# Kernel tuning notes

Measured on AMD Instinct MI355X. Metric: run time of the kernel, lower is better.

The kernel has to match this reference:

```python
import jax, jax.numpy as jnp
import numpy as np

LBL = 20            # original label_size
T = LBL + 2         # +START/+STOP for CRF
START = T - 2
STOP = T - 1
B, S, V, E, H = 64, 256, 50000, 300, 256


def setup_inputs() -> dict:
    key = jax.random.key(0)
    ks = jax.random.split(key, 20)
    s = 0.05
    inp = {
        "word_input": jax.random.randint(ks[0], (B, S), 0, V),
        "input_mask": jnp.ones((B, S), dtype=jnp.int32),
        "labels": jax.random.randint(ks[1], (B, S), 0, LBL),
        "labels_token": jax.random.randint(ks[2], (B, S), 0, 2),
        "emb_table": jax.random.normal(ks[3], (V, E)) * s,
        # PyTorch LSTM gate order: i, f, g, o (stacked along dim 0 of W)
        "Wih_f": jax.random.normal(ks[4], (4 * H, E)) * s,
        "Whh_f": jax.random.normal(ks[5], (4 * H, H)) * s,
        "bih_f": jax.random.normal(ks[6], (4 * H,)) * s,
        "bhh_f": jax.random.normal(ks[7], (4 * H,)) * s,
        "Wih_b": jax.random.normal(ks[8], (4 * H, E)) * s,
        "Whh_b": jax.random.normal(ks[9], (4 * H, H)) * s,
        "bih_b": jax.random.normal(ks[10], (4 * H,)) * s,
        "bhh_b": jax.random.normal(ks[11], (4 * H,)) * s,
        "W_tag": jax.random.normal(ks[12], (T, 2 * H)) * s,
        "b_tag": jax.random.normal(ks[13], (T,)) * s,
        "W_tok": jax.random.normal(ks[14], (2, 2 * H)) * s,
        "b_tok": jax.random.normal(ks[15], (2,)) * s,
        "trans": jax.random.normal(ks[16], (T, T)) * 0.1,
    }
    return inp


def _lstm_dir(x, Wih, Whh, bih, bhh, reverse):
    # x: [B, S, E] -> hs: [B, S, H]
    b = x.shape[0]
    h0 = jnp.zeros((b, Whh.shape[1]), x.dtype)

    def step(carry, xt):
        h, c = carry
        g = xt @ Wih.T + bih + h @ Whh.T + bhh
        i, f, gg, o = jnp.split(g, 4, axis=-1)
        c = jax.nn.sigmoid(f) * c + jax.nn.sigmoid(i) * jnp.tanh(gg)
        h = jax.nn.sigmoid(o) * jnp.tanh(c)
        return (h, c), h

    _, hs = jax.lax.scan(step, (h0, h0), jnp.swapaxes(x, 0, 1), reverse=reverse)
    return jnp.swapaxes(hs, 0, 1)


def _crf_nll(feats, mask, tags, trans):
    # feats: [B,S,T], mask: [B,S] int, tags: [B,S]
    maskf = mask.astype(feats.dtype)
    feats_t = jnp.swapaxes(feats, 0, 1)  # [S,B,T]
    mask_t = jnp.swapaxes(mask, 0, 1)
    part0 = feats_t[0] + trans[START][None]  # [B,T]

    def step(part, inputs):
        ft, mt = inputs
        newp = jax.nn.logsumexp(part[:, :, None] + trans[None], axis=1) + ft
        return jnp.where(mt[:, None] > 0, newp, part), None

    part, _ = jax.lax.scan(step, part0, (feats_t[1:], mask_t[1:]))
    fwd = jax.nn.logsumexp(part + trans[:, STOP][None], axis=1).sum()

    prev = jnp.concatenate(
        [jnp.full((tags.shape[0], 1), START, dtype=tags.dtype), tags[:, :-1]], axis=1)
    emit = jnp.take_along_axis(feats, tags[:, :, None], axis=2)[:, :, 0]
    gold = ((emit + trans[prev, tags]) * maskf).sum()
    lengths = mask.sum(axis=1)
    last_tag = jnp.take_along_axis(tags, (lengths - 1)[:, None], axis=1)[:, 0]
    gold = gold + trans[last_tag, STOP].sum()
    return fwd - gold


def _viterbi(feats, mask, trans):
    feats_t = jnp.swapaxes(feats, 0, 1)
    mask_t = jnp.swapaxes(mask, 0, 1)
    vit0 = feats_t[0] + trans[START][None]  # [B,T]
    idT = jnp.arange(T)

    def step(vit, inputs):
        ft, mt = inputs
        sc = vit[:, :, None] + trans[None]       # [B, T_prev, T_cur]
        bp = jnp.argmax(sc, axis=1)
        newv = jnp.max(sc, axis=1) + ft
        vit = jnp.where(mt[:, None] > 0, newv, vit)
        bp = jnp.where(mt[:, None] > 0, bp, idT[None])  # identity at padding
        return vit, bp

    vit, bps = jax.lax.scan(step, vit0, (feats_t[1:], mask_t[1:]))  # bps: [S-1,B,T]
    final = vit + trans[:, STOP][None]
    score = jnp.max(final, axis=1)
    last = jnp.argmax(final, axis=1)

    def back(tag, bp):
        prev = jnp.take_along_axis(bp, tag[:, None], axis=1)[:, 0]
        return prev, prev

    _, prevs = jax.lax.scan(back, last, bps, reverse=True)  # [S-1,B]
    tags = jnp.concatenate([prevs, last[None]], axis=0)      # [S,B]
    return score, jnp.swapaxes(tags, 0, 1)


def reference(word_input, input_mask, labels, labels_token, emb_table,
              Wih_f, Whh_f, bih_f, bhh_f, Wih_b, Whh_b, bih_b, bhh_b,
              W_tag, b_tag, W_tok, b_tok, trans):
    x = emb_table[word_input]                                  # [B,S,E]
    x = x * input_mask[:, :, None].astype(x.dtype)
    h_f = _lstm_dir(x, Wih_f, Whh_f, bih_f, bhh_f, reverse=False)
    h_b = _lstm_dir(x, Wih_b, Whh_b, bih_b, bhh_b, reverse=True)
    output = jnp.concatenate([h_f, h_b], axis=-1)              # [B,S,2H]

    tag_feats = output @ W_tag.T + b_tag                       # [B,S,T]
    tok_logits = output @ W_tok.T + b_tok                      # [B,S,2]

    # token CE: active positions (mask==1) and ignore_index=0
    logp = jax.nn.log_softmax(tok_logits, axis=-1)
    ce = -jnp.take_along_axis(logp, labels_token[:, :, None], axis=2)[:, :, 0]
    w = ((input_mask == 1) & (labels_token != 0)).astype(ce.dtype)
    token_loss = (ce * w).sum() / jnp.maximum(w.sum(), 1.0)

    nll = _crf_nll(tag_feats, input_mask, labels, trans)
    scores, tag_seq = _viterbi(tag_feats, input_mask, trans)
    ans_loss = nll / word_input.shape[0] + token_loss
    return ans_loss, tag_seq
```

## Files before the change

kernel.cpp:

```cpp
#include <hip/hip_runtime.h>
#include <math.h>

typedef unsigned short u16;
typedef unsigned int u32;

#define NB 64
#define NS 256
#define NE 300
#define NH 256
#define NT 22
#define KPAD 304
#define NBS (NB*NS)
#define START_TAG 20
#define STOP_TAG 21

#define RKC 20
#define LDSC 9
#define SKC 35

typedef float f32x4 __attribute__((ext_vector_type(4)));

__device__ __forceinline__ float fsig(float x) {
    return 1.f / (1.f + expf(-x));
}

__global__ __launch_bounds__(128) void gather_ax(const int* __restrict__ word,
                                                 const int* __restrict__ mask,
                                                 const float* __restrict__ emb,
                                                 float* __restrict__ Ax) {
    int bs = blockIdx.x;
    int t = threadIdx.x;
    if (t >= 76) return;
    int w = word[bs];
    int m = mask[bs];
    f32x4 v = {0.f, 0.f, 0.f, 0.f};
    if (t < 75 && m != 0) v = *(const f32x4*)(emb + (size_t)w * NE + t * 4);
    *(f32x4*)(Ax + (size_t)bs * KPAD + t * 4) = v;
}

__global__ __launch_bounds__(64) void pack_wih(const float* __restrict__ Wf, const float* __restrict__ Wb,
                                               const float* __restrict__ bihf, const float* __restrict__ bhhf,
                                               const float* __restrict__ bihb, const float* __restrict__ bhhb,
                                               float* __restrict__ WihP, float* __restrict__ biasP) {
    int j = blockIdx.x & 1023;
    int dir = blockIdx.x >> 10;
    const float* W = dir ? Wb : Wf;
    for (int k = threadIdx.x; k < KPAD; k += 64)
        WihP[((size_t)dir * 1024 + j) * KPAD + k] = (k < NE) ? W[(size_t)j * NE + k] : 0.f;
    if (threadIdx.x == 0) {
        const float* b1 = dir ? bihb : bihf;
        const float* b2 = dir ? bhhb : bhhf;
        biasP[dir * 1024 + j] = b1[j] + b2[j];
    }
}

__global__ __launch_bounds__(256) void pack_wstream(const float* __restrict__ Whf,
                                                    const float* __restrict__ Whb,
                                                    float* __restrict__ Wst) {
    int idx = blockIdx.x * 256 + threadIdx.x;
    int dir = idx / (SKC * 1024);
    int r = idx % (SKC * 1024);
    int cc = r >> 10;
    int row = r & 1023;
    const float* W = dir ? Whb : Whf;
    f32x4 v = *(const f32x4*)(W + (size_t)row * NH + 4 * (RKC + LDSC + cc));
    *((f32x4*)Wst + idx) = v;
}

__global__ __launch_bounds__(256) void gemm_xproj(const float* __restrict__ Ax,
                                                  const float* __restrict__ WihP,
                                                  const float* __restrict__ biasP,
                                                  float* __restrict__ Xp) {
    int m0 = blockIdx.x * 128;
    int n0 = blockIdx.y * 64;
    int dir = blockIdx.z;
    const float* Bsrc = WihP + (size_t)dir * 1024 * KPAD;
    __shared__ float Asm[16][132];
    __shared__ float Bsm[16][68];
    int tid = threadIdx.x;
    int arow = tid >> 1;
    int acol = (tid & 1) * 8;
    int brow = tid >> 2;
    int bcol = (tid & 3) * 4;
    int ty = tid >> 4;
    int tx = tid & 15;
    float acc[8][4] = {};

    for (int ks = 0; ks < KPAD / 16; ++ks) {
        int k0 = ks * 16;
        f32x4 ga0 = *(const f32x4*)(Ax + (size_t)(m0 + arow) * KPAD + k0 + acol);
        f32x4 ga1 = *(const f32x4*)(Ax + (size_t)(m0 + arow) * KPAD + k0 + acol + 4);
        f32x4 gb = *(const f32x4*)(Bsrc + (size_t)(n0 + brow) * KPAD + k0 + bcol);
        __syncthreads();
#pragma unroll
        for (int j = 0; j < 4; ++j) {
            Asm[acol + j][arow] = ga0[j];
            Asm[acol + 4 + j][arow] = ga1[j];
            Bsm[bcol + j][brow] = gb[j];
        }
        __syncthreads();
#pragma unroll
        for (int k = 0; k < 16; ++k) {
            f32x4 a0 = *(const f32x4*)&Asm[k][ty * 8];
            f32x4 a1 = *(const f32x4*)&Asm[k][ty * 8 + 4];
            f32x4 b4 = *(const f32x4*)&Bsm[k][tx * 4];
#pragma unroll
            for (int i = 0; i < 4; ++i)
#pragma unroll
                for (int j = 0; j < 4; ++j) {
                    acc[i][j] = fmaf(a0[i], b4[j], acc[i][j]);
                    acc[i + 4][j] = fmaf(a1[i], b4[j], acc[i + 4][j]);
                }
        }
    }
    f32x4 bv = *(const f32x4*)(biasP + dir * 1024 + n0 + tx * 4);
#pragma unroll
    for (int i = 0; i < 8; ++i) {
        f32x4 o;
#pragma unroll
        for (int j = 0; j < 4; ++j) o[j] = acc[i][j] + bv[j];
        *(f32x4*)(Xp + ((size_t)dir * NBS + m0 + ty * 8 + i) * 1024 + n0 + tx * 4) = o;
    }
}

__global__ __launch_bounds__(1024, 4) void lstm5(const float* __restrict__ Xp,
                                                 const float* __restrict__ Whf,
                                                 const float* __restrict__ Whb,
                                                 const float* __restrict__ Wst,
                                                 float* __restrict__ hbuf) {
    int bid = blockIdx.x;
    int dir = bid >> 6;
    int b = bid & 63;
    int tid = threadIdx.x;
    int gate = tid >> 8;
    int j = tid & 255;
    __shared__ f32x4 wlds[LDSC][1024];
    __shared__ float h_sh[256];
    __shared__ float exch[3][256];

    const float* W = dir ? Whb : Whf;
    const f32x4* wrow = (const f32x4*)(W + (size_t)tid * NH);
    const f32x4* ws = (const f32x4*)Wst + (size_t)dir * SKC * 1024;

    f32x4 wr[RKC];
#pragma unroll
    for (int i = 0; i < RKC; ++i) wr[i] = wrow[i];
#pragma unroll
    for (int i = 0; i < LDSC; ++i) wlds[i][tid] = wrow[RKC + i];

    const float* X = Xp + ((size_t)dir * NBS + (size_t)b * NS) * 1024;
    float* Hout = hbuf + ((size_t)dir * NBS + (size_t)b * NS) * NH;
    const f32x4* hs4 = (const f32x4*)h_sh;
    float c = 0.f;
    if (gate == 0) h_sh[j] = 0.f;
    __syncthreads();

    for (int t = 0; t < NS; ++t) {
        int s = dir ? (NS - 1 - t) : t;
        float acc = X[(size_t)s * 1024 + tid];
#pragma unroll 5
        for (int cc = 0; cc < SKC; ++cc) {
            f32x4 wv = ws[(size_t)cc * 1024 + tid];
            f32x4 hq = hs4[RKC + LDSC + cc];
            acc = fmaf(wv[0], hq[0], fmaf(wv[1], hq[1], fmaf(wv[2], hq[2], fmaf(wv[3], hq[3], acc))));
        }
#pragma unroll
        for (int i = 0; i < RKC; ++i) {
            f32x4 hq = hs4[i];
            acc = fmaf(wr[i][0], hq[0], fmaf(wr[i][1], hq[1], fmaf(wr[i][2], hq[2], fmaf(wr[i][3], hq[3], acc))));
        }
#pragma unroll
        for (int i = 0; i < LDSC; ++i) {
            f32x4 wv = wlds[i][tid];
            f32x4 hq = hs4[RKC + i];
            acc = fmaf(wv[0], hq[0], fmaf(wv[1], hq[1], fmaf(wv[2], hq[2], fmaf(wv[3], hq[3], acc))));
        }
        if (gate) exch[gate - 1][j] = (gate == 2) ? tanhf(acc) : fsig(acc);
        __syncthreads();
        if (!gate) {
            float gi = fsig(acc);
            float gf = exch[0][j];
            float gg = exch[1][j];
            float oo = exch[2][j];
            c = gf * c + gi * gg;
            float h = oo * tanhf(c);
            h_sh[j] = h;
            Hout[(size_t)s * NH + j] = h;
        }
        __syncthreads();
    }
}

__global__ __launch_bounds__(256) void feats_kernel(const float* __restrict__ hbuf,
                                                    const float* __restrict__ Wtag, const float* __restrict__ btag,
                                                    const float* __restrict__ Wtok, const float* __restrict__ btok,
                                                    const int* __restrict__ mask, const int* __restrict__ ltok,
                                                    float* __restrict__ feats,
                                                    float* __restrict__ ce_arr, float* __restrict__ cnt_arr) {
    int gw = (blockIdx.x * 256 + threadIdx.x) >> 6;
    int lane = threadIdx.x & 63;
    float ce = 0.f, cnt = 0.f;
    for (int i = 0; i < 8; ++i) {
        int bs = gw * 8 + i;
        size_t base = (lane < 32) ? ((size_t)bs * NH + lane * 8)
                                  : ((size_t)NBS * NH + (size_t)bs * NH + (lane - 32) * 8);
        f32x4 v0 = *(const f32x4*)(hbuf + base);
        f32x4 v1 = *(const f32x4*)(hbuf + base + 4);
        float vals[8] = {v0[0], v0[1], v0[2], v0[3], v1[0], v1[1], v1[2], v1[3]};
        float t0 = 0.f, t1 = 0.f;
        for (int u = 0; u < 24; ++u) {
            const float* wr = (u < NT) ? (Wtag + (size_t)u * 512) : (Wtok + (size_t)(u - NT) * 512);
            f32x4 w0 = *(const f32x4*)(wr + lane * 8);
            f32x4 w1 = *(const f32x4*)(wr + lane * 8 + 4);
            float d = vals[0] * w0[0] + vals[1] * w0[1] + vals[2] * w0[2] + vals[3] * w0[3]
                    + vals[4] * w1[0] + vals[5] * w1[1] + vals[6] * w1[2] + vals[7] * w1[3];
#pragma unroll
            for (int o = 32; o; o >>= 1) d += __shfl_xor(d, o);
            if (u < NT) {
                if (lane == 0) feats[(size_t)bs * 24 + u] = d + btag[u];
            } else if (u == NT) {
                t0 = d + btok[0];
            } else {
                t1 = d + btok[1];
            }
        }
        if (lane == 0) {
            float m = fmaxf(t0, t1);
            float lse = m + logf(expf(t0 - m) + expf(t1 - m));
            int lab = ltok[bs];
            int mk = mask[bs];
            if (mk == 1 && lab != 0) {
                ce += lse - (lab ? t1 : t0);
                cnt += 1.f;
            }
        }
    }
    if (lane == 0) { ce_arr[gw] = ce; cnt_arr[gw] = cnt; }
}

__global__ __launch_bounds__(64) void crf_kernel(const float* __restrict__ feats,
                                                 const int* __restrict__ mask,
                                                 const int* __restrict__ labels,
                                                 const float* __restrict__ trans,
                                                 float* __restrict__ contrib,
                                                 float* __restrict__ outtags) {
    int b = blockIdx.x, t = threadIdx.x;
    __shared__ float tr[NT * NT];
    __shared__ float part_sh[NT], vit_sh[NT];
    __shared__ float red[NT];
    __shared__ unsigned char bp[NS][NT];
    for (int i = t; i < NT * NT; i += 64) tr[i] = trans[i];
    __syncthreads();
    const float* F = feats + (size_t)b * NS * 24;
    const int* Mrow = mask + b * NS;
    const int* Lrow = labels + b * NS;
    float part = 0.f, vit = 0.f;
    if (t < NT) {
        part = F[t] + tr[START_TAG * NT + t];
        vit = part;
        part_sh[t] = part;
        vit_sh[t] = vit;
    }
    __syncthreads();
    for (int s = 1; s < NS; ++s) {
        float newp = part, newv = vit;
        int bi = t;
        if (t < NT) {
            float ft = F[s * 24 + t];
            float mx = -1e30f;
#pragma unroll
            for (int p = 0; p < NT; ++p) mx = fmaxf(mx, part_sh[p] + tr[p * NT + t]);
            float sm = 0.f;
#pragma unroll
            for (int p = 0; p < NT; ++p) sm += expf(part_sh[p] + tr[p * NT + t] - mx);
            float cp = mx + logf(sm) + ft;
            float bm = -1e30f;
            int bj = 0;
#pragma unroll
            for (int p = 0; p < NT; ++p) {
                float sc = vit_sh[p] + tr[p * NT + t];
                if (sc > bm) { bm = sc; bj = p; }
            }
            float cv = bm + ft;
            if (Mrow[s] > 0) { newp = cp; newv = cv; bi = bj; }
        }
        __syncthreads();
        if (t < NT) {
            part = newp; vit = newv;
            part_sh[t] = part; vit_sh[t] = vit;
            bp[s][t] = (unsigned char)bi;
        }
        __syncthreads();
    }
    float val = (t < NT) ? part + tr[t * NT + STOP_TAG] : -1e30f;
    float mx = val;
#pragma unroll
    for (int o = 32; o; o >>= 1) mx = fmaxf(mx, __shfl_xor(mx, o));
    float ex = (t < NT) ? expf(val - mx) : 0.f;
#pragma unroll
    for (int o = 32; o; o >>= 1) ex += __shfl_xor(ex, o);
    float fwd = mx + logf(ex);
    if (t < NT) red[t] = vit + tr[t * NT + STOP_TAG];
    __syncthreads();
    if (t == 0) {
        float bm = -1e30f;
        int bi = 0;
        for (int p = 0; p < NT; ++p)
            if (red[p] > bm) { bm = red[p]; bi = p; }
        int cur = bi;
        outtags[b * NS + NS - 1] = (float)cur;
        for (int s = NS - 1; s >= 1; --s) {
            cur = bp[s][cur];
            outtags[b * NS + s - 1] = (float)cur;
        }
    }
    float g = 0.f;
    int len = 0;
    for (int s = t; s < NS; s += 64) {
        int tg = Lrow[s];
        int pv = (s == 0) ? START_TAG : Lrow[s - 1];
        if (Mrow[s] > 0) {
            g += F[s * 24 + tg] + tr[pv * NT + tg];
            len += 1;
        }
    }
#pragma unroll
    for (int o = 32; o; o >>= 1) { g += __shfl_xor(g, o); len += __shfl_xor(len, o); }
    if (t == 0) {
        int lt = Lrow[len - 1];
        g += tr[lt * NT + STOP_TAG];
        contrib[b] = fwd - g;
    }
}

__global__ __launch_bounds__(256) void finalize_kernel(const float* __restrict__ contrib,
                                                       const float* __restrict__ ce_arr,
                                                       const float* __restrict__ cnt_arr,
                                                       float* __restrict__ out) {
    __shared__ float sA[256], sB[256], sC[256];
    int t = threadIdx.x;
    float a = (t < NB) ? contrib[t] : 0.f;
    float bb = 0.f, cc = 0.f;
    for (int i = t; i < 2048; i += 256) { bb += ce_arr[i]; cc += cnt_arr[i]; }
    sA[t] = a; sB[t] = bb; sC[t] = cc;
    __syncthreads();
    for (int o = 128; o; o >>= 1) {
        if (t < o) { sA[t] += sA[t + o]; sB[t] += sB[t + o]; sC[t] += sC[t + o]; }
        __syncthreads();
    }
    if (t == 0)
        out[0] = sA[0] / (float)NB + sB[0] / fmaxf(sC[0], 1.f);
}

extern "C" void kernel_launch(void* const* d_in, const int* in_sizes, int n_in,
                              void* d_out, int out_size, void* d_ws, size_t ws_size,
                              hipStream_t stream) {
    const int*   word   = (const int*)d_in[0];
    const int*   mask   = (const int*)d_in[1];
    const int*   labels = (const int*)d_in[2];
    const int*   ltok   = (const int*)d_in[3];
    const float* emb    = (const float*)d_in[4];
    const float* Wih_f  = (const float*)d_in[5];
    const float* Whh_f  = (const float*)d_in[6];
    const float* bih_f  = (const float*)d_in[7];
    const float* bhh_f  = (const float*)d_in[8];
    const float* Wih_b  = (const float*)d_in[9];
    const float* Whh_b  = (const float*)d_in[10];
    const float* bih_b  = (const float*)d_in[11];
    const float* bhh_b  = (const float*)d_in[12];
    const float* Wtag   = (const float*)d_in[13];
    const float* btag   = (const float*)d_in[14];
    const float* Wtok   = (const float*)d_in[15];
    const float* btok   = (const float*)d_in[16];
    const float* trans  = (const float*)d_in[17];
    float* out = (float*)d_out;

    char* ws = (char*)d_ws;
    size_t off = 0;
    auto alloc = [&](size_t bytes) { size_t r = off; off += (bytes + 255) & ~(size_t)255; return r; };
    float* Ax     = (float*)(ws + alloc((size_t)NBS * KPAD * 4));
    float* WihP   = (float*)(ws + alloc((size_t)2 * 1024 * KPAD * 4));
    float* biasP  = (float*)(ws + alloc((size_t)2 * 1024 * 4));
    float* Wst    = (float*)(ws + alloc((size_t)2 * SKC * 1024 * 16));
    float* Xp     = (float*)(ws + alloc((size_t)2 * NBS * 1024 * 4));
    float* hbuf   = (float*)(ws + alloc((size_t)2 * NBS * NH * 4));
    float* feats  = (float*)(ws + alloc((size_t)NBS * 24 * 4));
    float* contrib= (float*)(ws + alloc((size_t)NB * 4));
    float* ce_arr = (float*)(ws + alloc((size_t)2048 * 4));
    float* cnt_arr= (float*)(ws + alloc((size_t)2048 * 4));

    gather_ax<<<NBS, 128, 0, stream>>>(word, mask, emb, Ax);
    pack_wih<<<2048, 64, 0, stream>>>(Wih_f, Wih_b, bih_f, bhh_f, bih_b, bhh_b, WihP, biasP);
    pack_wstream<<<(2 * SKC * 1024) / 256, 256, 0, stream>>>(Whh_f, Whh_b, Wst);
    gemm_xproj<<<dim3(NBS / 128, 1024 / 64, 2), 256, 0, stream>>>(Ax, WihP, biasP, Xp);
    lstm5<<<128, 1024, 0, stream>>>(Xp, Whh_f, Whh_b, Wst, hbuf);
    feats_kernel<<<512, 256, 0, stream>>>(hbuf, Wtag, btag, Wtok, btok, mask, ltok, feats, ce_arr, cnt_arr);
    crf_kernel<<<NB, 64, 0, stream>>>(feats, mask, labels, trans, contrib, out + 1);
    finalize_kernel<<<1, 256, 0, stream>>>(contrib, ce_arr, cnt_arr, out);
}
```

Before: 2.246 ms.

## Fuse embedding gather into input GEMM and repack recurrent weights chunk-major

Removes the separate embedding gather kernel and its padded intermediate buffer: the input-projection GEMM now reads embedding rows directly, applying the mask and zero padding as it loads. The recurrent weights are repacked fully chunk-major so every per-thread load in the LSTM is coalesced. The register/stream split is shifted (fewer register chunks, more streamed chunks), with an asm barrier pinning the weights in VGPRs and a smaller unroll. The trade is more streamed weight traffic per timestep in the sequential LSTM loop, in exchange for lower register pressure and one fewer launch.

```diff
diff --git a/kernel.cpp b/kernel.cpp
--- a/kernel.cpp
+++ b/kernel.cpp
@@ -14,28 +14,14 @@
 #define START_TAG 20
 #define STOP_TAG 21
 
-#define RKC 20
+#define RKC 18
 #define LDSC 9
-#define SKC 35
+#define SKC 37
 
 typedef float f32x4 __attribute__((ext_vector_type(4)));
 
 __device__ __forceinline__ float fsig(float x) {
     return 1.f / (1.f + expf(-x));
-}
-
-__global__ __launch_bounds__(128) void gather_ax(const int* __restrict__ word,
-                                                 const int* __restrict__ mask,
-                                                 const float* __restrict__ emb,
-                                                 float* __restrict__ Ax) {
-    int bs = blockIdx.x;
-    int t = threadIdx.x;
-    if (t >= 76) return;
-    int w = word[bs];
-    int m = mask[bs];
-    f32x4 v = {0.f, 0.f, 0.f, 0.f};
-    if (t < 75 && m != 0) v = *(const f32x4*)(emb + (size_t)w * NE + t * 4);
-    *(f32x4*)(Ax + (size_t)bs * KPAD + t * 4) = v;
 }
 
 __global__ __launch_bounds__(64) void pack_wih(const float* __restrict__ Wf, const float* __restrict__ Wb,
@@ -54,20 +40,22 @@
     }
 }
 
-__global__ __launch_bounds__(256) void pack_wstream(const float* __restrict__ Whf,
-                                                    const float* __restrict__ Whb,
-                                                    float* __restrict__ Wst) {
+__global__ __launch_bounds__(256) void pack_wall(const float* __restrict__ Whf,
+                                                 const float* __restrict__ Whb,
+                                                 float* __restrict__ WstAll) {
     int idx = blockIdx.x * 256 + threadIdx.x;
-    int dir = idx / (SKC * 1024);
-    int r = idx % (SKC * 1024);
+    int dir = idx >> 16;
+    int r = idx & 65535;
     int cc = r >> 10;
     int row = r & 1023;
     const float* W = dir ? Whb : Whf;
-    f32x4 v = *(const f32x4*)(W + (size_t)row * NH + 4 * (RKC + LDSC + cc));
-    *((f32x4*)Wst + idx) = v;
-}
-
-__global__ __launch_bounds__(256) void gemm_xproj(const float* __restrict__ Ax,
+    f32x4 v = *(const f32x4*)(W + (size_t)row * NH + 4 * cc);
+    *((f32x4*)WstAll + idx) = v;
+}
+
+__global__ __launch_bounds__(256) void gemm_xproj(const int* __restrict__ word,
+                                                  const int* __restrict__ maskp,
+                                                  const float* __restrict__ emb,
                                                   const float* __restrict__ WihP,
                                                   const float* __restrict__ biasP,
                                                   float* __restrict__ Xp) {
@@ -86,10 +74,17 @@
     int tx = tid & 15;
     float acc[8][4] = {};
 
+    int bs = m0 + arow;
+    int wi = word[bs];
+    int mk = maskp[bs];
+    const float* erow = emb + (size_t)wi * NE;
+
     for (int ks = 0; ks < KPAD / 16; ++ks) {
         int k0 = ks * 16;
-        f32x4 ga0 = *(const f32x4*)(Ax + (size_t)(m0 + arow) * KPAD + k0 + acol);
-        f32x4 ga1 = *(const f32x4*)(Ax + (size_t)(m0 + arow) * KPAD + k0 + acol + 4);
+        int c0 = k0 + acol;
+        f32x4 ga0 = {0.f, 0.f, 0.f, 0.f}, ga1 = {0.f, 0.f, 0.f, 0.f};
+        if (mk && c0 < NE)     ga0 = *(const f32x4*)(erow + c0);
+        if (mk && c0 + 4 < NE) ga1 = *(const f32x4*)(erow + c0 + 4);
         f32x4 gb = *(const f32x4*)(Bsrc + (size_t)(n0 + brow) * KPAD + k0 + bcol);
         __syncthreads();
 #pragma unroll
@@ -123,10 +118,8 @@
     }
 }
 
-__global__ __launch_bounds__(1024, 4) void lstm5(const float* __restrict__ Xp,
-                                                 const float* __restrict__ Whf,
-                                                 const float* __restrict__ Whb,
-                                                 const float* __restrict__ Wst,
+__global__ __launch_bounds__(1024, 4) void lstm6(const float* __restrict__ Xp,
+                                                 const float* __restrict__ WstAll,
                                                  float* __restrict__ hbuf) {
     int bid = blockIdx.x;
     int dir = bid >> 6;
@@ -138,16 +131,18 @@
     __shared__ float h_sh[256];
     __shared__ float exch[3][256];
 
-    const float* W = dir ? Whb : Whf;
-    const f32x4* wrow = (const f32x4*)(W + (size_t)tid * NH);
-    const f32x4* ws = (const f32x4*)Wst + (size_t)dir * SKC * 1024;
+    const f32x4* wall = (const f32x4*)WstAll + (size_t)dir * 64 * 1024;
 
     f32x4 wr[RKC];
 #pragma unroll
-    for (int i = 0; i < RKC; ++i) wr[i] = wrow[i];
-#pragma unroll
-    for (int i = 0; i < LDSC; ++i) wlds[i][tid] = wrow[RKC + i];
-
+    for (int i = 0; i < RKC; ++i) wr[i] = wall[(size_t)i * 1024 + tid];
+#pragma unroll
+    for (int i = 0; i < RKC; ++i)
+        asm volatile("" : "+v"(wr[i][0]), "+v"(wr[i][1]), "+v"(wr[i][2]), "+v"(wr[i][3]));
+#pragma unroll
+    for (int i = 0; i < LDSC; ++i) wlds[i][tid] = wall[(size_t)(RKC + i) * 1024 + tid];
+
+    const f32x4* ws = wall + (size_t)(RKC + LDSC) * 1024;
     const float* X = Xp + ((size_t)dir * NBS + (size_t)b * NS) * 1024;
     float* Hout = hbuf + ((size_t)dir * NBS + (size_t)b * NS) * NH;
     const f32x4* hs4 = (const f32x4*)h_sh;
@@ -158,7 +153,7 @@
     for (int t = 0; t < NS; ++t) {
         int s = dir ? (NS - 1 - t) : t;
         float acc = X[(size_t)s * 1024 + tid];
-#pragma unroll 5
+#pragma unroll 4
         for (int cc = 0; cc < SKC; ++cc) {
             f32x4 wv = ws[(size_t)cc * 1024 + tid];
             f32x4 hq = hs4[RKC + LDSC + cc];
@@ -378,10 +373,9 @@
     char* ws = (char*)d_ws;
     size_t off = 0;
     auto alloc = [&](size_t bytes) { size_t r = off; off += (bytes + 255) & ~(size_t)255; return r; };
-    float* Ax     = (float*)(ws + alloc((size_t)NBS * KPAD * 4));
     float* WihP   = (float*)(ws + alloc((size_t)2 * 1024 * KPAD * 4));
     float* biasP  = (float*)(ws + alloc((size_t)2 * 1024 * 4));
-    float* Wst    = (float*)(ws + alloc((size_t)2 * SKC * 1024 * 16));
+    float* WstAll = (float*)(ws + alloc((size_t)2 * 64 * 1024 * 16));
     float* Xp     = (float*)(ws + alloc((size_t)2 * NBS * 1024 * 4));
     float* hbuf   = (float*)(ws + alloc((size_t)2 * NBS * NH * 4));
     float* feats  = (float*)(ws + alloc((size_t)NBS * 24 * 4));
@@ -389,11 +383,10 @@
     float* ce_arr = (float*)(ws + alloc((size_t)2048 * 4));
     float* cnt_arr= (float*)(ws + alloc((size_t)2048 * 4));
 
-    gather_ax<<<NBS, 128, 0, stream>>>(word, mask, emb, Ax);
     pack_wih<<<2048, 64, 0, stream>>>(Wih_f, Wih_b, bih_f, bhh_f, bih_b, bhh_b, WihP, biasP);
-    pack_wstream<<<(2 * SKC * 1024) / 256, 256, 0, stream>>>(Whh_f, Whh_b, Wst);
-    gemm_xproj<<<dim3(NBS / 128, 1024 / 64, 2), 256, 0, stream>>>(Ax, WihP, biasP, Xp);
-    lstm5<<<128, 1024, 0, stream>>>(Xp, Whh_f, Whh_b, Wst, hbuf);
+    pack_wall<<<512, 256, 0, stream>>>(Whh_f, Whh_b, WstAll);
+    gemm_xproj<<<dim3(NBS / 128, 1024 / 64, 2), 256, 0, stream>>>(word, mask, emb, WihP, biasP, Xp);
+    lstm6<<<128, 1024, 0, stream>>>(Xp, WstAll, hbuf);
     feats_kernel<<<512, 256, 0, stream>>>(hbuf, Wtag, btag, Wtok, btok, mask, ltok, feats, ce_arr, cnt_arr);
     crf_kernel<<<NB, 64, 0, stream>>>(feats, mask, labels, trans, contrib, out + 1);
     finalize_kernel<<<1, 256, 0, stream>>>(contrib, ce_arr, cnt_arr, out);
```

After: 2.379 ms. 1.06x slower.

## Fuse embedding gather into input GEMM, enlarge tile, sync-free wave-per-batch CRF

Applied to the files above, without the earlier changes.

Removes the separate embedding gather kernel and its intermediate buffer by loading embedding rows directly inside the input-projection GEMM, with masking and K padding handled in-kernel. The GEMM tile is widened to 128x128 so each thread computes 8x8 outputs, giving more reuse per shared-memory load. The CRF/Viterbi kernel now assigns one wavefront per batch row, four per block, and drops block-level barriers in the sequential recurrence. It relies on intra-wavefront lockstep for correctness of the shared-memory updates.

```diff
diff --git a/kernel.cpp b/kernel.cpp
--- a/kernel.cpp
+++ b/kernel.cpp
@@ -22,20 +22,6 @@
 
 __device__ __forceinline__ float fsig(float x) {
     return 1.f / (1.f + expf(-x));
-}
-
-__global__ __launch_bounds__(128) void gather_ax(const int* __restrict__ word,
-                                                 const int* __restrict__ mask,
-                                                 const float* __restrict__ emb,
-                                                 float* __restrict__ Ax) {
-    int bs = blockIdx.x;
-    int t = threadIdx.x;
-    if (t >= 76) return;
-    int w = word[bs];
-    int m = mask[bs];
-    f32x4 v = {0.f, 0.f, 0.f, 0.f};
-    if (t < 75 && m != 0) v = *(const f32x4*)(emb + (size_t)w * NE + t * 4);
-    *(f32x4*)(Ax + (size_t)bs * KPAD + t * 4) = v;
 }
 
 __global__ __launch_bounds__(64) void pack_wih(const float* __restrict__ Wf, const float* __restrict__ Wb,
@@ -67,59 +53,74 @@
     *((f32x4*)Wst + idx) = v;
 }
 
-__global__ __launch_bounds__(256) void gemm_xproj(const float* __restrict__ Ax,
-                                                  const float* __restrict__ WihP,
-                                                  const float* __restrict__ biasP,
-                                                  float* __restrict__ Xp) {
+__global__ __launch_bounds__(256, 4) void gemm_xproj(const int* __restrict__ word,
+                                                     const int* __restrict__ maskp,
+                                                     const float* __restrict__ emb,
+                                                     const float* __restrict__ WihP,
+                                                     const float* __restrict__ biasP,
+                                                     float* __restrict__ Xp) {
     int m0 = blockIdx.x * 128;
-    int n0 = blockIdx.y * 64;
+    int n0 = blockIdx.y * 128;
     int dir = blockIdx.z;
     const float* Bsrc = WihP + (size_t)dir * 1024 * KPAD;
     __shared__ float Asm[16][132];
-    __shared__ float Bsm[16][68];
+    __shared__ float Bsm[16][132];
     int tid = threadIdx.x;
     int arow = tid >> 1;
     int acol = (tid & 1) * 8;
-    int brow = tid >> 2;
-    int bcol = (tid & 3) * 4;
     int ty = tid >> 4;
     int tx = tid & 15;
-    float acc[8][4] = {};
+    float acc[8][8] = {};
+
+    int bs = m0 + arow;
+    int wi = word[bs];
+    int mk = maskp[bs];
+    const float* erow = emb + (size_t)wi * NE;
 
     for (int ks = 0; ks < KPAD / 16; ++ks) {
         int k0 = ks * 16;
-        f32x4 ga0 = *(const f32x4*)(Ax + (size_t)(m0 + arow) * KPAD + k0 + acol);
-        f32x4 ga1 = *(const f32x4*)(Ax + (size_t)(m0 + arow) * KPAD + k0 + acol + 4);
-        f32x4 gb = *(const f32x4*)(Bsrc + (size_t)(n0 + brow) * KPAD + k0 + bcol);
+        int c0 = k0 + acol;
+        f32x4 ga0 = {0.f, 0.f, 0.f, 0.f}, ga1 = {0.f, 0.f, 0.f, 0.f};
+        if (mk && c0 < NE)     ga0 = *(const f32x4*)(erow + c0);
+        if (mk && c0 + 4 < NE) ga1 = *(const f32x4*)(erow + c0 + 4);
+        f32x4 gb0 = *(const f32x4*)(Bsrc + (size_t)(n0 + arow) * KPAD + c0);
+        f32x4 gb1 = *(const f32x4*)(Bsrc + (size_t)(n0 + arow) * KPAD + c0 + 4);
         __syncthreads();
 #pragma unroll
         for (int j = 0; j < 4; ++j) {
             Asm[acol + j][arow] = ga0[j];
             Asm[acol + 4 + j][arow] = ga1[j];
-            Bsm[bcol + j][brow] = gb[j];
+            Bsm[acol + j][arow] = gb0[j];
+            Bsm[acol + 4 + j][arow] = gb1[j];
         }
         __syncthreads();
 #pragma unroll
         for (int k = 0; k < 16; ++k) {
             f32x4 a0 = *(const f32x4*)&Asm[k][ty * 8];
             f32x4 a1 = *(const f32x4*)&Asm[k][ty * 8 + 4];
-            f32x4 b4 = *(const f32x4*)&Bsm[k][tx * 4];
+            f32x4 b0 = *(const f32x4*)&Bsm[k][tx * 8];
+            f32x4 b1 = *(const f32x4*)&Bsm[k][tx * 8 + 4];
 #pragma unroll
             for (int i = 0; i < 4; ++i)
 #pragma unroll
                 for (int j = 0; j < 4; ++j) {
-                    acc[i][j] = fmaf(a0[i], b4[j], acc[i][j]);
-                    acc[i + 4][j] = fmaf(a1[i], b4[j], acc[i + 4][j]);
+                    acc[i][j]         = fmaf(a0[i], b0[j], acc[i][j]);
+                    acc[i][j + 4]     = fmaf(a0[i], b1[j], acc[i][j + 4]);
+                    acc[i + 4][j]     = fmaf(a1[i], b0[j], acc[i + 4][j]);
+                    acc[i + 4][j + 4] = fmaf(a1[i], b1[j], acc[i + 4][j + 4]);
                 }
         }
     }
-    f32x4 bv = *(const f32x4*)(biasP + dir * 1024 + n0 + tx * 4);
+    f32x4 bv0 = *(const f32x4*)(biasP + dir * 1024 + n0 + tx * 8);
+    f32x4 bv1 = *(const f32x4*)(biasP + dir * 1024 + n0 + tx * 8 + 4);
 #pragma unroll
     for (int i = 0; i < 8; ++i) {
-        f32x4 o;
-#pragma unroll
-        for (int j = 0; j < 4; ++j) o[j] = acc[i][j] + bv[j];
-        *(f32x4*)(Xp + ((size_t)dir * NBS + m0 + ty * 8 + i) * 1024 + n0 + tx * 4) = o;
+        f32x4 o0, o1;
+#pragma unroll
+        for (int j = 0; j < 4; ++j) { o0[j] = acc[i][j] + bv0[j]; o1[j] = acc[i][j + 4] + bv1[j]; }
+        float* dst = Xp + ((size_t)dir * NBS + m0 + ty * 8 + i) * 1024 + n0 + tx * 8;
+        *(f32x4*)dst = o0;
+        *(f32x4*)(dst + 4) = o1;
     }
 }
 
@@ -238,59 +239,57 @@
     if (lane == 0) { ce_arr[gw] = ce; cnt_arr[gw] = cnt; }
 }
 
-__global__ __launch_bounds__(64) void crf_kernel(const float* __restrict__ feats,
-                                                 const int* __restrict__ mask,
-                                                 const int* __restrict__ labels,
-                                                 const float* __restrict__ trans,
-                                                 float* __restrict__ contrib,
-                                                 float* __restrict__ outtags) {
-    int b = blockIdx.x, t = threadIdx.x;
+__global__ __launch_bounds__(256) void crf_kernel(const float* __restrict__ feats,
+                                                  const int* __restrict__ mask,
+                                                  const int* __restrict__ labels,
+                                                  const float* __restrict__ trans,
+                                                  float* __restrict__ contrib,
+                                                  float* __restrict__ outtags) {
+    int wid = threadIdx.x >> 6;
+    int lane = threadIdx.x & 63;
+    int b = blockIdx.x * 4 + wid;
     __shared__ float tr[NT * NT];
-    __shared__ float part_sh[NT], vit_sh[NT];
-    __shared__ float red[NT];
-    __shared__ unsigned char bp[NS][NT];
-    for (int i = t; i < NT * NT; i += 64) tr[i] = trans[i];
+    __shared__ float ps[4][NT], vs[4][NT];
+    __shared__ unsigned char bp[4][NS][NT];
+    for (int i = threadIdx.x; i < NT * NT; i += 256) tr[i] = trans[i];
     __syncthreads();
+
     const float* F = feats + (size_t)b * NS * 24;
     const int* Mrow = mask + b * NS;
     const int* Lrow = labels + b * NS;
+    int t = lane;
     float part = 0.f, vit = 0.f;
     if (t < NT) {
         part = F[t] + tr[START_TAG * NT + t];
         vit = part;
-        part_sh[t] = part;
-        vit_sh[t] = vit;
-    }
-    __syncthreads();
+        ps[wid][t] = part;
+        vs[wid][t] = vit;
+    }
     for (int s = 1; s < NS; ++s) {
-        float newp = part, newv = vit;
-        int bi = t;
+        int mt = Mrow[s];
         if (t < NT) {
             float ft = F[s * 24 + t];
-            float mx = -1e30f;
-#pragma unroll
-            for (int p = 0; p < NT; ++p) mx = fmaxf(mx, part_sh[p] + tr[p * NT + t]);
+            float mx = -1e30f, bm = -1e30f;
+            int bj = 0;
+#pragma unroll
+            for (int p = 0; p < NT; ++p) {
+                float a = ps[wid][p] + tr[p * NT + t];
+                mx = fmaxf(mx, a);
+                float v = vs[wid][p] + tr[p * NT + t];
+                if (v > bm) { bm = v; bj = p; }
+            }
             float sm = 0.f;
 #pragma unroll
-            for (int p = 0; p < NT; ++p) sm += expf(part_sh[p] + tr[p * NT + t] - mx);
+            for (int p = 0; p < NT; ++p)
+                sm += expf(ps[wid][p] + tr[p * NT + t] - mx);
             float cp = mx + logf(sm) + ft;
-            float bm = -1e30f;
-            int bj = 0;
-#pragma unroll
-            for (int p = 0; p < NT; ++p) {
-                float sc = vit_sh[p] + tr[p * NT + t];
-                if (sc > bm) { bm = sc; bj = p; }
-            }
             float cv = bm + ft;
-            if (Mrow[s] > 0) { newp = cp; newv = cv; bi = bj; }
-        }
-        __syncthreads();
-        if (t < NT) {
-            part = newp; vit = newv;
-            part_sh[t] = part; vit_sh[t] = vit;
-            bp[s][t] = (unsigned char)bi;
-        }
-        __syncthreads();
+            int bi = t;
+            if (mt > 0) { part = cp; vit = cv; bi = bj; }
+            bp[wid][s][t] = (unsigned char)bi;
+            ps[wid][t] = part;
+            vs[wid][t] = vit;
+        }
     }
     float val = (t < NT) ? part + tr[t * NT + STOP_TAG] : -1e30f;
     float mx = val;
@@ -300,23 +299,23 @@
 #pragma unroll
     for (int o = 32; o; o >>= 1) ex += __shfl_xor(ex, o);
     float fwd = mx + logf(ex);
-    if (t < NT) red[t] = vit + tr[t * NT + STOP_TAG];
-    __syncthreads();
-    if (t == 0) {
+    if (lane == 0) {
         float bm = -1e30f;
         int bi = 0;
-        for (int p = 0; p < NT; ++p)
-            if (red[p] > bm) { bm = red[p]; bi = p; }
+        for (int p = 0; p < NT; ++p) {
+            float sc = vs[wid][p] + tr[p * NT + STOP_TAG];
+            if (sc > bm) { bm = sc; bi = p; }
+        }
         int cur = bi;
         outtags[b * NS + NS - 1] = (float)cur;
         for (int s = NS - 1; s >= 1; --s) {
-            cur = bp[s][cur];
+            cur = bp[wid][s][cur];
             outtags[b * NS + s - 1] = (float)cur;
         }
     }
     float g = 0.f;
     int len = 0;
-    for (int s = t; s < NS; s += 64) {
+    for (int s = lane; s < NS; s += 64) {
         int tg = Lrow[s];
         int pv = (s == 0) ? START_TAG : Lrow[s - 1];
         if (Mrow[s] > 0) {
@@ -326,7 +325,7 @@
     }
 #pragma unroll
     for (int o = 32; o; o >>= 1) { g += __shfl_xor(g, o); len += __shfl_xor(len, o); }
-    if (t == 0) {
+    if (lane == 0) {
         int lt = Lrow[len - 1];
         g += tr[lt * NT + STOP_TAG];
         contrib[b] = fwd - g;
@@ -378,7 +377,6 @@
     char* ws = (char*)d_ws;
     size_t off = 0;
     auto alloc = [&](size_t bytes) { size_t r = off; off += (bytes + 255) & ~(size_t)255; return r; };
-    float* Ax     = (float*)(ws + alloc((size_t)NBS * KPAD * 4));
     float* WihP   = (float*)(ws + alloc((size_t)2 * 1024 * KPAD * 4));
     float* biasP  = (float*)(ws + alloc((size_t)2 * 1024 * 4));
     float* Wst    = (float*)(ws + alloc((size_t)2 * SKC * 1024 * 16));
@@ -389,12 +387,11 @@
     float* ce_arr = (float*)(ws + alloc((size_t)2048 * 4));
     float* cnt_arr= (float*)(ws + alloc((size_t)2048 * 4));
 
-    gather_ax<<<NBS, 128, 0, stream>>>(word, mask, emb, Ax);
     pack_wih<<<2048, 64, 0, stream>>>(Wih_f, Wih_b, bih_f, bhh_f, bih_b, bhh_b, WihP, biasP);
     pack_wstream<<<(2 * SKC * 1024) / 256, 256, 0, stream>>>(Whh_f, Whh_b, Wst);
-    gemm_xproj<<<dim3(NBS / 128, 1024 / 64, 2), 256, 0, stream>>>(Ax, WihP, biasP, Xp);
+    gemm_xproj<<<dim3(NBS / 128, 1024 / 128, 2), 256, 0, stream>>>(word, mask, emb, WihP, biasP, Xp);
     lstm5<<<128, 1024, 0, stream>>>(Xp, Whh_f, Whh_b, Wst, hbuf);
     feats_kernel<<<512, 256, 0, stream>>>(hbuf, Wtag, btag, Wtok, btok, mask, ltok, feats, ce_arr, cnt_arr);
-    crf_kernel<<<NB, 64, 0, stream>>>(feats, mask, labels, trans, contrib, out + 1);
+    crf_kernel<<<NB / 4, 256, 0, stream>>>(feats, mask, labels, trans, contrib, out + 1);
     finalize_kernel<<<1, 256, 0, stream>>>(contrib, ce_arr, cnt_arr, out);
 }
```

After: 2.404 ms. +7.0%, slower.
